# Kernel tuning notes

Measured on AMD Instinct MI355X. Metric: run time of the kernel, lower is better.

The kernel has to match this reference:

```python
import jax, jax.numpy as jnp
import numpy as np

N = 8192       # subgraph nodes
F_IN = 512     # input feature dim
F_OUT = 256    # hidden dim (hardcoded 256 in fit())
M = 4096       # masked output nodes
DENSITY = 0.01
NEG_SLOPE = 0.01  # nn.LeakyReLU default


def setup_inputs() -> dict:
    key = jax.random.key(0)
    k_adj, k_feat, k_w, k_a1, k_a2, k_mask = jax.random.split(key, 6)
    adj = (jax.random.uniform(k_adj, (N, N)) < DENSITY).astype(jnp.float32)
    adj = jnp.maximum(adj, jnp.eye(N, dtype=jnp.float32))  # self-loops (sampler always adds them)
    eye = jnp.eye(N, dtype=jnp.float32)
    feats = jax.random.normal(k_feat, (N, F_IN), dtype=jnp.float32)
    W = jax.random.normal(k_w, (F_OUT, F_IN), dtype=jnp.float32) * (1.0 / np.sqrt(F_IN))
    b = jnp.zeros((F_OUT,), dtype=jnp.float32)
    a_1 = jax.random.uniform(k_a1, (1, F_OUT), dtype=jnp.float32)
    a_2 = jax.random.uniform(k_a2, (1, F_OUT), dtype=jnp.float32)
    node_mask = jax.random.randint(k_mask, (M,), 0, N)
    return {"adj_matrix": adj, "eye_matrix": eye, "subgraph_feats": feats,
            "node_mask": node_mask, "W": W, "b": b, "a_1": a_1, "a_2": a_2}


def reference(adj_matrix, eye_matrix, subgraph_feats, node_mask, W, b, a_1, a_2):
    z = subgraph_feats @ W.T + b                         # [N, F_OUT]
    zi = jnp.sum(a_1 * z, axis=1, keepdims=True)         # [N, 1]
    zj = jnp.sum(a_2 * z, axis=1, keepdims=True)         # [N, 1]
    att = adj_matrix * zi + adj_matrix * (eye_matrix * zj)  # [N, N]
    att = jnp.exp(jax.nn.leaky_relu(att, NEG_SLOPE)) * adj_matrix
    att = att / jnp.sum(att, axis=1, keepdims=True)      # row-normalize
    h = z - att @ z                                      # residual subtract aggregate
    return jax.nn.relu(h[node_mask])                     # [M, F_OUT]
```

## Files before the change

### kernel.cpp

```cpp
#include <hip/hip_runtime.h>
#include <hip/hip_bf16.h>


typedef float  f32x4  __attribute__((ext_vector_type(4)));
typedef short  s16x8  __attribute__((ext_vector_type(8)));
typedef unsigned short u16x4 __attribute__((ext_vector_type(4)));

#define KDIM  512
#define NODES 8192
#define FOUT  256
#define MOUT  4096

static __device__ inline unsigned short f2bf(float f) {
    union { float f; unsigned u; } x; x.f = f;
    unsigned r = x.u + 0x7FFFu + ((x.u >> 16) & 1u);
    return (unsigned short)(r >> 16);
}
static __device__ inline float bf2f(unsigned short u) {
    union { unsigned u; float f; } x; x.u = ((unsigned)u) << 16;
    return x.f;
}

static __device__ inline void gload_lds16(const void* g, void* l) {
    __builtin_amdgcn_global_load_lds(
        (const __attribute__((address_space(1))) unsigned int*)g,
        (__attribute__((address_space(3))) unsigned int*)l, 16, 0, 0);
}

#define FEAT_G (NODES * KDIM / 8)
#define W_G    (FOUT * KDIM / 8)
__global__ __launch_bounds__(256) void to_bf16(
    const float* __restrict__ feats, const float* __restrict__ W,
    unsigned short* __restrict__ fb, unsigned short* __restrict__ wb)
{
    const int t = blockIdx.x * 256 + threadIdx.x;
    const float* src;
    unsigned short* dst;
    if (t < FEAT_G) { src = feats + (size_t)t * 8; dst = fb + (size_t)t * 8; }
    else           { const int u = t - FEAT_G; src = W + (size_t)u * 8; dst = wb + (size_t)u * 8; }
    const f32x4 a = *(const f32x4*)src;
    const f32x4 b = *(const f32x4*)(src + 4);
    s16x8 p;
    #pragma unroll
    for (int j = 0; j < 4; j++) { p[j] = (short)f2bf(a[j]); p[4 + j] = (short)f2bf(b[j]); }
    *(s16x8*)dst = p;
}

__global__ __launch_bounds__(256) void gemm_z(
    const unsigned short* __restrict__ fb,
    const unsigned short* __restrict__ wb,
    const float* __restrict__ bias,
    float* __restrict__ zf,
    unsigned short* __restrict__ zb)
{
    __shared__ unsigned short lA[128 * 32];
    __shared__ unsigned short lB[128 * 32];

    const int tid  = threadIdx.x;
    const int lane = tid & 63;
    const int wave = tid >> 6;
    const int quad = lane >> 4;
    const int l16  = lane & 15;
    const int bm = blockIdx.x;
    const int bn = blockIdx.y;
    const int wr = wave >> 1, wc = wave & 1;

    f32x4 acc[4][4] = {};

    const int rowA = tid >> 2;
    const int c8   = tid & 3;
    const unsigned short* gA = fb + (size_t)(bm * 128 + rowA) * KDIM + c8 * 8;
    const unsigned short* gB = wb + (size_t)(bn * 128 + rowA) * KDIM + c8 * 8;
    char* dA = (char*)lA + tid * 16;
    char* dB = (char*)lB + tid * 16;

    for (int kt = 0; kt < KDIM; kt += 32) {
        __syncthreads();
        gload_lds16(gA + kt,            dA);
        gload_lds16(gA + kt + 64 * KDIM, dA + 4096);
        gload_lds16(gB + kt,            dB);
        gload_lds16(gB + kt + 64 * KDIM, dB + 4096);
        __syncthreads();

        s16x8 af[4], bfr[4];
        #pragma unroll
        for (int mi = 0; mi < 4; mi++)
            af[mi] = *(const s16x8*)&lA[(wr * 64 + mi * 16 + l16) * 32 + quad * 8];
        #pragma unroll
        for (int ni = 0; ni < 4; ni++)
            bfr[ni] = *(const s16x8*)&lB[(wc * 64 + ni * 16 + l16) * 32 + quad * 8];
        #pragma unroll
        for (int mi = 0; mi < 4; mi++)
            #pragma unroll
            for (int ni = 0; ni < 4; ni++)
                acc[mi][ni] = __builtin_amdgcn_mfma_f32_16x16x32_bf16(
                    af[mi], bfr[ni], acc[mi][ni], 0, 0, 0);
    }

    #pragma unroll
    for (int ni = 0; ni < 4; ni++) {
        const int gcol = bn * 128 + wc * 64 + ni * 16 + l16;
        const float bv = bias[gcol];
        #pragma unroll
        for (int mi = 0; mi < 4; mi++) {
            const int grow0 = bm * 128 + wr * 64 + mi * 16 + quad * 4;
            #pragma unroll
            for (int rr = 0; rr < 4; rr++) {
                const float v = acc[mi][ni][rr] + bv;
                const size_t off = (size_t)(grow0 + rr) * FOUT + gcol;
                zf[off] = v;
                zb[off] = f2bf(v);
            }
        }
    }
}

#define IDX_CAP 512

__global__ __launch_bounds__(256) void attn_rows(
    const float* __restrict__ adj,
    const int*   __restrict__ mask,
    const float* __restrict__ zf,
    const unsigned short* __restrict__ zb,
    const float* __restrict__ a1,
    const float* __restrict__ a2,
    float* __restrict__ out)
{
    __shared__ int   s_idx[4][IDX_CAP];
    __shared__ int   s_cnt[4];
    __shared__ float s_red[2][4];
    __shared__ float s_S[4][FOUT];

    const int tid  = threadIdx.x;
    const int lane = tid & 63;
    const int wave = tid >> 6;
    const int m    = blockIdx.x;
    const int row  = mask[m];

    const float zt = zf[(size_t)row * FOUT + tid];
    float p1 = a1[tid] * zt;
    float p2 = a2[tid] * zt;
    #pragma unroll
    for (int off = 32; off; off >>= 1) {
        p1 += __shfl_xor(p1, off);
        p2 += __shfl_xor(p2, off);
    }
    if (lane == 0) { s_red[0][wave] = p1; s_red[1][wave] = p2; }

    int cnt = 0;
    const float* arow = adj + (size_t)row * NODES + wave * 2048;
    #pragma unroll
    for (int c = 0; c < 2048; c += 256) {
        const f32x4 v = *(const f32x4*)(arow + c + 4 * lane);
        #pragma unroll
        for (int t = 0; t < 4; t++) {
            const bool nz = (v[t] != 0.0f);
            const unsigned long long mk = __ballot(nz);
            const int pre = __popcll(mk & ((1ull << lane) - 1ull));
            if (nz) {
                const int slot = cnt + pre;
                if (slot < IDX_CAP)
                    s_idx[wave][slot] = wave * 2048 + c + 4 * lane + t;
            }
            cnt += __popcll(mk);
        }
    }
    if (lane == 0) s_cnt[wave] = cnt;
    __syncthreads();

    const int deg = s_cnt[0] + s_cnt[1] + s_cnt[2] + s_cnt[3];

    f32x4 S = {0.f, 0.f, 0.f, 0.f};
    const int myc = s_cnt[wave];
    int i = 0;
    for (; i + 4 <= myc; i += 4) {
        const int j0 = s_idx[wave][i + 0];
        const int j1 = s_idx[wave][i + 1];
        const int j2 = s_idx[wave][i + 2];
        const int j3 = s_idx[wave][i + 3];
        const u16x4 z0 = *(const u16x4*)(zb + (size_t)j0 * FOUT + 4 * lane);
        const u16x4 z1 = *(const u16x4*)(zb + (size_t)j1 * FOUT + 4 * lane);
        const u16x4 z2 = *(const u16x4*)(zb + (size_t)j2 * FOUT + 4 * lane);
        const u16x4 z3 = *(const u16x4*)(zb + (size_t)j3 * FOUT + 4 * lane);
        #pragma unroll
        for (int t = 0; t < 4; t++)
            S[t] += bf2f(z0[t]) + bf2f(z1[t]) + bf2f(z2[t]) + bf2f(z3[t]);
    }
    for (; i < myc; i++) {
        const int j = s_idx[wave][i];
        const u16x4 zn = *(const u16x4*)(zb + (size_t)j * FOUT + 4 * lane);
        #pragma unroll
        for (int t = 0; t < 4; t++) S[t] += bf2f(zn[t]);
    }
    *(f32x4*)&s_S[wave][4 * lane] = S;
    __syncthreads();

    if (wave == 0) {
        f32x4 St = *(const f32x4*)&s_S[0][4 * lane];
        #pragma unroll
        for (int w = 1; w < 4; w++) {
            const f32x4 Sw = *(const f32x4*)&s_S[w][4 * lane];
            #pragma unroll
            for (int t = 0; t < 4; t++) St[t] += Sw[t];
        }
        const float zi = s_red[0][0] + s_red[0][1] + s_red[0][2] + s_red[0][3];
        const float zj = s_red[1][0] + s_red[1][1] + s_red[1][2] + s_red[1][3];

        const float li = zi > 0.f ? zi : 0.01f * zi;
        const float sd = zi + zj;
        const float ld = sd > 0.f ? sd : 0.01f * sd;
        const float e_off  = expf(li);
        const float e_diag = expf(ld);
        const float denom  = (float)(deg - 1) * e_off + e_diag;
        const float w_off  = e_off / denom;
        const float w_d    = e_diag / denom;
        const float coef   = 1.0f + w_off - w_d;

        const f32x4 zr = *(const f32x4*)(zf + (size_t)row * FOUT + 4 * lane);
        f32x4 h;
        #pragma unroll
        for (int t = 0; t < 4; t++) {
            const float hv = zr[t] * coef - w_off * St[t];
            h[t] = hv > 0.f ? hv : 0.f;
        }
        *(f32x4*)(out + (size_t)m * FOUT + 4 * lane) = h;
    }
}

extern "C" void kernel_launch(void* const* d_in, const int* in_sizes, int n_in,
                              void* d_out, int out_size, void* d_ws, size_t ws_size,
                              hipStream_t stream)
{
    const float* adj   = (const float*)d_in[0];
    const float* feats = (const float*)d_in[2];
    const int*   mask  = (const int*)d_in[3];
    const float* W     = (const float*)d_in[4];
    const float* bias  = (const float*)d_in[5];
    const float* a1    = (const float*)d_in[6];
    const float* a2    = (const float*)d_in[7];
    float* out = (float*)d_out;

    char* ws = (char*)d_ws;
    float*          zf = (float*)          (ws);
    unsigned short* zb = (unsigned short*) (ws + 8388608);
    unsigned short* fb = (unsigned short*) (ws + 12582912);
    unsigned short* wb = (unsigned short*) (ws + 20971520);

    to_bf16<<<dim3((FEAT_G + W_G) / 256), dim3(256), 0, stream>>>(feats, W, fb, wb);
    gemm_z<<<dim3(NODES / 128, FOUT / 128), dim3(256), 0, stream>>>(fb, wb, bias, zf, zb);
    attn_rows<<<dim3(MOUT), dim3(256), 0, stream>>>(adj, mask, zf, zb, a1, a2, out);
}
```

Baseline: 470.4 us.

## Hoist adjacency scan into conversion kernel and build per-row neighbor lists

The scan of masked adjacency rows moves out of the attention kernel into the first launch, which now also does the bf16 conversion of features and weights. Each wave scans one full row and writes a compact neighbor index list and a degree count to workspace. The final kernel then handles four output rows per block, one per wave, reads the precomputed list to gather z and applies the softmax-weighted residual with no LDS and no block barriers. This lets the bandwidth-heavy scan run alongside the conversion and off the GEMM's critical path, and it removes cross-wave reductions. The cost is an extra global round trip for the index lists, and a single wave now walks a whole 8192-wide row, which gives less memory parallelism per row.

```diff
diff --git a/kernel.cpp b/kernel.cpp
--- a/kernel.cpp
+++ b/kernel.cpp
@@ -10,6 +10,7 @@
 #define NODES 8192
 #define FOUT  256
 #define MOUT  4096
+#define CAP   192
 
 static __device__ inline unsigned short f2bf(float f) {
     union { float f; unsigned u; } x; x.f = f;
@@ -27,23 +28,58 @@
         (__attribute__((address_space(3))) unsigned int*)l, 16, 0, 0);
 }
 
+#define SCAN_BLOCKS 1024
 #define FEAT_G (NODES * KDIM / 8)
 #define W_G    (FOUT * KDIM / 8)
-__global__ __launch_bounds__(256) void to_bf16(
+#define CONV_BLOCKS ((FEAT_G + W_G) / 256)
+
+__global__ __launch_bounds__(256) void scan_and_convert(
+    const float* __restrict__ adj,
+    const int*   __restrict__ mask,
+    int*   __restrict__ nbr,
+    int*   __restrict__ deg,
     const float* __restrict__ feats, const float* __restrict__ W,
     unsigned short* __restrict__ fb, unsigned short* __restrict__ wb)
 {
-    const int t = blockIdx.x * 256 + threadIdx.x;
-    const float* src;
-    unsigned short* dst;
-    if (t < FEAT_G) { src = feats + (size_t)t * 8; dst = fb + (size_t)t * 8; }
-    else           { const int u = t - FEAT_G; src = W + (size_t)u * 8; dst = wb + (size_t)u * 8; }
-    const f32x4 a = *(const f32x4*)src;
-    const f32x4 b = *(const f32x4*)(src + 4);
-    s16x8 p;
-    #pragma unroll
-    for (int j = 0; j < 4; j++) { p[j] = (short)f2bf(a[j]); p[4 + j] = (short)f2bf(b[j]); }
-    *(s16x8*)dst = p;
+    const int tid = threadIdx.x;
+    if (blockIdx.x < SCAN_BLOCKS) {
+        const int lane = tid & 63;
+        const int wave = tid >> 6;
+        const int m    = blockIdx.x * 4 + wave;
+        const int row  = mask[m];
+        const float* arow = adj + (size_t)row * NODES;
+        int* list = nbr + (size_t)m * CAP;
+        const unsigned long long below = (1ull << lane) - 1ull;
+
+        int cnt = 0;
+        #pragma unroll 4
+        for (int c = 0; c < NODES; c += 256) {
+            const f32x4 v = *(const f32x4*)(arow + c + 4 * lane);
+            #pragma unroll
+            for (int t = 0; t < 4; t++) {
+                const bool nz = (v[t] != 0.0f);
+                const unsigned long long mk = __ballot(nz);
+                if (nz) {
+                    const int slot = cnt + __popcll(mk & below);
+                    if (slot < CAP) list[slot] = c + 4 * lane + t;
+                }
+                cnt += __popcll(mk);
+            }
+        }
+        if (lane == 0) deg[m] = cnt;
+    } else {
+        const int t = (blockIdx.x - SCAN_BLOCKS) * 256 + tid;
+        const float* src;
+        unsigned short* dst;
+        if (t < FEAT_G) { src = feats + (size_t)t * 8; dst = fb + (size_t)t * 8; }
+        else            { const int u = t - FEAT_G; src = W + (size_t)u * 8; dst = wb + (size_t)u * 8; }
+        const f32x4 a = *(const f32x4*)src;
+        const f32x4 b = *(const f32x4*)(src + 4);
+        s16x8 p;
+        #pragma unroll
+        for (int j = 0; j < 4; j++) { p[j] = (short)f2bf(a[j]); p[4 + j] = (short)f2bf(b[j]); }
+        *(s16x8*)dst = p;
+    }
 }
 
 __global__ __launch_bounds__(256) void gemm_z(
@@ -76,9 +112,9 @@
 
     for (int kt = 0; kt < KDIM; kt += 32) {
         __syncthreads();
-        gload_lds16(gA + kt,            dA);
+        gload_lds16(gA + kt,             dA);
         gload_lds16(gA + kt + 64 * KDIM, dA + 4096);
-        gload_lds16(gB + kt,            dB);
+        gload_lds16(gB + kt,             dB);
         gload_lds16(gB + kt + 64 * KDIM, dB + 4096);
         __syncthreads();
 
@@ -115,10 +151,9 @@
     }
 }
 
-#define IDX_CAP 512
-
-__global__ __launch_bounds__(256) void attn_rows(
-    const float* __restrict__ adj,
+__global__ __launch_bounds__(256) void combine(
+    const int*   __restrict__ nbr,
+    const int*   __restrict__ deg,
     const int*   __restrict__ mask,
     const float* __restrict__ zf,
     const unsigned short* __restrict__ zb,
@@ -126,58 +161,32 @@
     const float* __restrict__ a2,
     float* __restrict__ out)
 {
-    __shared__ int   s_idx[4][IDX_CAP];
-    __shared__ int   s_cnt[4];
-    __shared__ float s_red[2][4];
-    __shared__ float s_S[4][FOUT];
-
-    const int tid  = threadIdx.x;
-    const int lane = tid & 63;
-    const int wave = tid >> 6;
-    const int m    = blockIdx.x;
+    const int lane = threadIdx.x & 63;
+    const int wave = threadIdx.x >> 6;
+    const int m    = blockIdx.x * 4 + wave;
     const int row  = mask[m];
 
-    const float zt = zf[(size_t)row * FOUT + tid];
-    float p1 = a1[tid] * zt;
-    float p2 = a2[tid] * zt;
+    const f32x4 zr  = *(const f32x4*)(zf + (size_t)row * FOUT + 4 * lane);
+    const f32x4 va1 = *(const f32x4*)(a1 + 4 * lane);
+    const f32x4 va2 = *(const f32x4*)(a2 + 4 * lane);
+
+    float zi = va1[0] * zr[0] + va1[1] * zr[1] + va1[2] * zr[2] + va1[3] * zr[3];
+    float zj = va2[0] * zr[0] + va2[1] * zr[1] + va2[2] * zr[2] + va2[3] * zr[3];
     #pragma unroll
     for (int off = 32; off; off >>= 1) {
-        p1 += __shfl_xor(p1, off);
-        p2 += __shfl_xor(p2, off);
-    }
-    if (lane == 0) { s_red[0][wave] = p1; s_red[1][wave] = p2; }
-
-    int cnt = 0;
-    const float* arow = adj + (size_t)row * NODES + wave * 2048;
-    #pragma unroll
-    for (int c = 0; c < 2048; c += 256) {
-        const f32x4 v = *(const f32x4*)(arow + c + 4 * lane);
-        #pragma unroll
-        for (int t = 0; t < 4; t++) {
-            const bool nz = (v[t] != 0.0f);
-            const unsigned long long mk = __ballot(nz);
-            const int pre = __popcll(mk & ((1ull << lane) - 1ull));
-            if (nz) {
-                const int slot = cnt + pre;
-                if (slot < IDX_CAP)
-                    s_idx[wave][slot] = wave * 2048 + c + 4 * lane + t;
-            }
-            cnt += __popcll(mk);
-        }
-    }
-    if (lane == 0) s_cnt[wave] = cnt;
-    __syncthreads();
-
-    const int deg = s_cnt[0] + s_cnt[1] + s_cnt[2] + s_cnt[3];
-
+        zi += __shfl_xor(zi, off);
+        zj += __shfl_xor(zj, off);
+    }
+
+    const int dg = deg[m];
+    const int* list = nbr + (size_t)m * CAP;
     f32x4 S = {0.f, 0.f, 0.f, 0.f};
-    const int myc = s_cnt[wave];
     int i = 0;
-    for (; i + 4 <= myc; i += 4) {
-        const int j0 = s_idx[wave][i + 0];
-        const int j1 = s_idx[wave][i + 1];
-        const int j2 = s_idx[wave][i + 2];
-        const int j3 = s_idx[wave][i + 3];
+    for (; i + 4 <= dg; i += 4) {
+        const int j0 = list[i + 0];
+        const int j1 = list[i + 1];
+        const int j2 = list[i + 2];
+        const int j3 = list[i + 3];
         const u16x4 z0 = *(const u16x4*)(zb + (size_t)j0 * FOUT + 4 * lane);
         const u16x4 z1 = *(const u16x4*)(zb + (size_t)j1 * FOUT + 4 * lane);
         const u16x4 z2 = *(const u16x4*)(zb + (size_t)j2 * FOUT + 4 * lane);
@@ -186,45 +195,30 @@
         for (int t = 0; t < 4; t++)
             S[t] += bf2f(z0[t]) + bf2f(z1[t]) + bf2f(z2[t]) + bf2f(z3[t]);
     }
-    for (; i < myc; i++) {
-        const int j = s_idx[wave][i];
+    for (; i < dg; i++) {
+        const int j = list[i];
         const u16x4 zn = *(const u16x4*)(zb + (size_t)j * FOUT + 4 * lane);
         #pragma unroll
         for (int t = 0; t < 4; t++) S[t] += bf2f(zn[t]);
     }
-    *(f32x4*)&s_S[wave][4 * lane] = S;
-    __syncthreads();
-
-    if (wave == 0) {
-        f32x4 St = *(const f32x4*)&s_S[0][4 * lane];
-        #pragma unroll
-        for (int w = 1; w < 4; w++) {
-            const f32x4 Sw = *(const f32x4*)&s_S[w][4 * lane];
-            #pragma unroll
-            for (int t = 0; t < 4; t++) St[t] += Sw[t];
-        }
-        const float zi = s_red[0][0] + s_red[0][1] + s_red[0][2] + s_red[0][3];
-        const float zj = s_red[1][0] + s_red[1][1] + s_red[1][2] + s_red[1][3];
-
-        const float li = zi > 0.f ? zi : 0.01f * zi;
-        const float sd = zi + zj;
-        const float ld = sd > 0.f ? sd : 0.01f * sd;
-        const float e_off  = expf(li);
-        const float e_diag = expf(ld);
-        const float denom  = (float)(deg - 1) * e_off + e_diag;
-        const float w_off  = e_off / denom;
-        const float w_d    = e_diag / denom;
-        const float coef   = 1.0f + w_off - w_d;
-
-        const f32x4 zr = *(const f32x4*)(zf + (size_t)row * FOUT + 4 * lane);
-        f32x4 h;
-        #pragma unroll
-        for (int t = 0; t < 4; t++) {
-            const float hv = zr[t] * coef - w_off * St[t];
-            h[t] = hv > 0.f ? hv : 0.f;
-        }
-        *(f32x4*)(out + (size_t)m * FOUT + 4 * lane) = h;
-    }
+
+    const float li = zi > 0.f ? zi : 0.01f * zi;
+    const float sd = zi + zj;
+    const float ld = sd > 0.f ? sd : 0.01f * sd;
+    const float e_off  = expf(li);
+    const float e_diag = expf(ld);
+    const float denom  = (float)(dg - 1) * e_off + e_diag;
+    const float w_off  = e_off / denom;
+    const float w_d    = e_diag / denom;
+    const float coef   = 1.0f + w_off - w_d;
+
+    f32x4 h;
+    #pragma unroll
+    for (int t = 0; t < 4; t++) {
+        const float hv = zr[t] * coef - w_off * S[t];
+        h[t] = hv > 0.f ? hv : 0.f;
+    }
+    *(f32x4*)(out + (size_t)m * FOUT + 4 * lane) = h;
 }
 
 extern "C" void kernel_launch(void* const* d_in, const int* in_sizes, int n_in,
@@ -241,12 +235,15 @@
     float* out = (float*)d_out;
 
     char* ws = (char*)d_ws;
-    float*          zf = (float*)          (ws);
-    unsigned short* zb = (unsigned short*) (ws + 8388608);
-    unsigned short* fb = (unsigned short*) (ws + 12582912);
-    unsigned short* wb = (unsigned short*) (ws + 20971520);
-
-    to_bf16<<<dim3((FEAT_G + W_G) / 256), dim3(256), 0, stream>>>(feats, W, fb, wb);
+    float*          zf  = (float*)          (ws);
+    unsigned short* zb  = (unsigned short*) (ws + 8388608);
+    unsigned short* fb  = (unsigned short*) (ws + 12582912);
+    unsigned short* wb  = (unsigned short*) (ws + 20971520);
+    int*            nbr = (int*)            (ws + 21233664);
+    int*            dg  = (int*)            (ws + 24379392);
+
+    scan_and_convert<<<dim3(SCAN_BLOCKS + CONV_BLOCKS), dim3(256), 0, stream>>>(
+        adj, mask, nbr, dg, feats, W, fb, wb);
     gemm_z<<<dim3(NODES / 128, FOUT / 128), dim3(256), 0, stream>>>(fb, wb, bias, zf, zb);
-    attn_rows<<<dim3(MOUT), dim3(256), 0, stream>>>(adj, mask, zf, zb, a1, a2, out);
-}
+    combine<<<dim3(MOUT / 4), dim3(256), 0, stream>>>(nbr, dg, mask, zf, zb, a1, a2, out);
+}
```

Result: no change. 479.1 us (+1.9%).
